# Optimization experiments

Hardware: AMD Instinct MI355X
Metric: run time of the kernel (lower is better)

Reference implementation:

```python
import jax, jax.numpy as jnp
import numpy as np

N_NODES = 100000
N_EDGES = 1600000
D_IN = 128
D_HID = 128
D_PROJ = 128
D_DEC = 512
BN_EPS = 1e-5
ENC_SLOPE = 0.5
DEC_SLOPE = 0.01


def _leaky(x, slope):
    return jnp.where(x >= 0, x, slope * x)


def setup_inputs() -> dict:
    key = jax.random.key(0)
    ks = jax.random.split(key, 12)
    glorot = lambda k, shp: jax.random.normal(k, shp, jnp.float32) * (1.0 / np.sqrt(shp[-1]))
    return {
        "x": jax.random.normal(ks[0], (N_NODES, D_IN), jnp.float32),
        "edge_index": jax.random.randint(ks[1], (2, N_EDGES), 0, N_NODES, jnp.int64),
        # SAGEConv: lin_l (neighbor aggr, with bias), lin_r (root, no bias)
        "Wl": glorot(ks[2], (D_HID, D_IN)),
        "bl": jnp.zeros((D_HID,), jnp.float32),
        "Wr": glorot(ks[3], (D_HID, D_IN)),
        # projection head: Linear + PReLU
        "Wp": glorot(ks[4], (D_PROJ, D_HID)),
        "bp": jnp.zeros((D_PROJ,), jnp.float32),
        "a_prelu": jnp.asarray(0.25, jnp.float32),
        # decoder: Linear -> BN -> LeakyReLU -> Linear
        "Wd1": glorot(ks[5], (D_DEC, D_HID)),
        "bd1": jnp.zeros((D_DEC,), jnp.float32),
        "gamma": jnp.ones((D_DEC,), jnp.float32),
        "beta": jnp.zeros((D_DEC,), jnp.float32),
        "Wd2": glorot(ks[6], (D_IN, D_DEC)),
        "bd2": jnp.zeros((D_IN,), jnp.float32),
    }


def reference(x, edge_index, Wl, bl, Wr, Wp, bp, a_prelu, Wd1, bd1, gamma, beta, Wd2, bd2):
    n = x.shape[0]
    src, dst = edge_index[0], edge_index[1]
    # SAGEConv mean aggregation: gather source features, segment-mean at dst
    msg_sum = jax.ops.segment_sum(x[src], dst, num_segments=n)   # [N, D_IN]
    cnt = jax.ops.segment_sum(jnp.ones((src.shape[0],), x.dtype), dst, num_segments=n)
    aggr = msg_sum / jnp.maximum(cnt, 1.0)[:, None]              # isolated nodes -> 0
    h = aggr @ Wl.T + bl + x @ Wr.T                              # lin_l(aggr) + lin_r(x)
    h = _leaky(h, ENC_SLOPE)                                     # encoder LeakyReLU(0.5)
    # projection head: Linear + PReLU
    zp = h @ Wp.T + bp
    z = jnp.where(zp >= 0, zp, a_prelu * zp)
    # decoder: Linear -> BatchNorm1d (training batch stats, biased var) -> LeakyReLU -> Linear
    d = h @ Wd1.T + bd1
    mu = jnp.mean(d, axis=0)
    var = jnp.mean(jnp.square(d - mu), axis=0)
    d = (d - mu) * jax.lax.rsqrt(var + BN_EPS) * gamma + beta
    d = _leaky(d, DEC_SLOPE)
    rec = d @ Wd2.T + bd2
    target = x
    return (h, z, rec, target)
```

## Files before the change

### kernel.cpp

```cpp
#include <hip/hip_runtime.h>
#include <cstdint>
#include <cstddef>

#define D 128
#define DDEC 512

typedef __attribute__((ext_vector_type(8))) short short8;
typedef __attribute__((ext_vector_type(4))) float f32x4;

__device__ __forceinline__ ushort f2bf(float f) {
  uint32_t u = __float_as_uint(f);
  u = u + 0x7FFF + ((u >> 16) & 1);
  return (ushort)(u >> 16);
}
__device__ __forceinline__ float bf2f(ushort u) {
  return __uint_as_float(((uint32_t)u) << 16);
}

__global__ void detect_i64(const int* __restrict__ ei, int* __restrict__ flag) {
  if (threadIdx.x == 0 && blockIdx.x == 0) {
    int allz = 1;
    for (int k = 0; k < 64; ++k)
      if (ei[2 * k + 1] != 0) { allz = 0; break; }
    *flag = allz ? 2 : 1;
  }
}

__global__ __launch_bounds__(256) void prep_count_kernel(
    const float* __restrict__ x, const float* __restrict__ Wl,
    const float* __restrict__ Wr, const float* __restrict__ Wp,
    const float* __restrict__ Wd1, const float* __restrict__ Wd2,
    const int* __restrict__ ei,
    ushort* __restrict__ xb, ushort* __restrict__ wb,
    float* __restrict__ tgt,
    int* __restrict__ deg, const int* __restrict__ flag,
    int n8, int xblocks, int E)
{
  int b = blockIdx.x;
  if (b < xblocks) {
    int i = b * 256 + threadIdx.x;
    if (i >= n8) return;
    const float* s = x + (size_t)i * 8;
    float4 f0 = *(const float4*)s;
    float4 f1 = *(const float4*)(s + 4);
    short8 v;
    v[0] = (short)f2bf(f0.x); v[1] = (short)f2bf(f0.y);
    v[2] = (short)f2bf(f0.z); v[3] = (short)f2bf(f0.w);
    v[4] = (short)f2bf(f1.x); v[5] = (short)f2bf(f1.y);
    v[6] = (short)f2bf(f1.z); v[7] = (short)f2bf(f1.w);
    *(short8*)&xb[(size_t)i * 8] = v;
    if (tgt) {
      *(float4*)&tgt[(size_t)i * 8] = f0;
      *(float4*)&tgt[(size_t)i * 8 + 4] = f1;
    }
  } else if (b < xblocks + 704) {
    int i = (b - xblocks) * 256 + threadIdx.x;
    if (i >= 180224) return;
    float v;
    if (i < 16384) v = Wl[i];
    else if (i < 32768) v = Wr[i - 16384];
    else if (i < 49152) v = Wp[i - 32768];
    else if (i < 114688) v = Wd1[i - 49152];
    else v = Wd2[i - 114688];
    wb[i] = f2bf(v);
  } else {
    int e = (b - xblocks - 704) * 256 + threadIdx.x;
    if (e >= E) return;
    int s = *flag;
    int dst = ei[((long long)E + e) * s];
    atomicAdd(&deg[dst], 1);
  }
}

__global__ __launch_bounds__(256) void scan_reduce(
    const int* __restrict__ deg, int* __restrict__ bsum, int N)
{
  __shared__ int red[256];
  int base = blockIdx.x * 1024 + threadIdx.x * 4;
  int s = 0;
#pragma unroll
  for (int k = 0; k < 4; ++k) { int i = base + k; if (i < N) s += deg[i]; }
  red[threadIdx.x] = s;
  __syncthreads();
  for (int off = 128; off > 0; off >>= 1) {
    if (threadIdx.x < off) red[threadIdx.x] += red[threadIdx.x + off];
    __syncthreads();
  }
  if (threadIdx.x == 0) bsum[blockIdx.x] = red[0];
}

__global__ void scan_bsum(int* __restrict__ bsum, int* __restrict__ rowptr,
                          int NB, int N, int E)
{
  __shared__ int tmp[256];
  int t = threadIdx.x;
  int v = (t < NB) ? bsum[t] : 0;
  tmp[t] = v;
  __syncthreads();
  for (int off = 1; off < 256; off <<= 1) {
    int add = (t >= off) ? tmp[t - off] : 0;
    __syncthreads();
    tmp[t] += add;
    __syncthreads();
  }
  if (t < NB) bsum[t] = tmp[t] - v;
  if (t == 0) rowptr[N] = E;
}

__global__ __launch_bounds__(256) void scan_final(
    const int* __restrict__ deg, const int* __restrict__ bsum,
    int* __restrict__ rowptr, int N)
{
  __shared__ int tsum[256];
  int base = blockIdx.x * 1024 + threadIdx.x * 4;
  int loc[4]; int s = 0;
#pragma unroll
  for (int k = 0; k < 4; ++k) { int i = base + k; loc[k] = (i < N) ? deg[i] : 0; s += loc[k]; }
  tsum[threadIdx.x] = s;
  __syncthreads();
  for (int off = 1; off < 256; off <<= 1) {
    int add = (threadIdx.x >= off) ? tsum[threadIdx.x - off] : 0;
    __syncthreads();
    tsum[threadIdx.x] += add;
    __syncthreads();
  }
  int excl = tsum[threadIdx.x] - s + bsum[blockIdx.x];
#pragma unroll
  for (int k = 0; k < 4; ++k) {
    int i = base + k;
    if (i < N) { rowptr[i] = excl; excl += loc[k]; }
  }
}

__global__ __launch_bounds__(256) void fill_csr(
    const int* __restrict__ ei, const int* __restrict__ rowptr,
    int* __restrict__ fillc, int* __restrict__ colidx,
    const int* __restrict__ flag, int E)
{
  int e = blockIdx.x * 256 + threadIdx.x;
  if (e >= E) return;
  int s = *flag;
  int src = ei[(long long)e * s];
  int dst = ei[((long long)E + e) * s];
  int pos = rowptr[dst] + atomicAdd(&fillc[dst], 1);
  colidx[pos] = src;
}

__global__ __launch_bounds__(256) void aggregate_kernel(
    const int* __restrict__ rowptr, const int* __restrict__ colidx,
    const ushort* __restrict__ xb, ushort* __restrict__ aggrb, int N)
{
  int wave = (blockIdx.x * 256 + threadIdx.x) >> 6;
  int lane = threadIdx.x & 63;
  if (wave >= N) return;
  int s = rowptr[wave], epos = rowptr[wave + 1];
  float ax = 0.f, ay = 0.f;
  int e = s;
  for (; e + 3 < epos; e += 4) {
    int s0 = colidx[e], s1 = colidx[e + 1], s2 = colidx[e + 2], s3 = colidx[e + 3];
    uint u0 = *(const uint*)&xb[(size_t)s0 * D + lane * 2];
    uint u1 = *(const uint*)&xb[(size_t)s1 * D + lane * 2];
    uint u2 = *(const uint*)&xb[(size_t)s2 * D + lane * 2];
    uint u3 = *(const uint*)&xb[(size_t)s3 * D + lane * 2];
    ax += __uint_as_float(u0 << 16) + __uint_as_float(u1 << 16)
        + __uint_as_float(u2 << 16) + __uint_as_float(u3 << 16);
    ay += __uint_as_float(u0 & 0xFFFF0000u) + __uint_as_float(u1 & 0xFFFF0000u)
        + __uint_as_float(u2 & 0xFFFF0000u) + __uint_as_float(u3 & 0xFFFF0000u);
  }
  for (; e < epos; ++e) {
    uint u0 = *(const uint*)&xb[(size_t)colidx[e] * D + lane * 2];
    ax += __uint_as_float(u0 << 16);
    ay += __uint_as_float(u0 & 0xFFFF0000u);
  }
  int degn = epos - s;
  float inv = 1.0f / (float)(degn > 0 ? degn : 1);
  uint out = ((uint)f2bf(ax * inv)) | (((uint)f2bf(ay * inv)) << 16);
  *(uint*)&aggrb[(size_t)wave * D + lane * 2] = out;
}

__device__ __forceinline__ void mma_tile_g(const ushort* __restrict__ A, size_t ald,
                                           const ushort* __restrict__ B, size_t bld,
                                           f32x4 acc[4][4], int lane)
{
  const int r = lane & 15, g = lane >> 4;
#pragma unroll
  for (int ks = 0; ks < 4; ++ks) {
    short8 a[4], b[4];
#pragma unroll
    for (int m = 0; m < 4; ++m)
      a[m] = *(const short8*)&A[(size_t)(m * 16 + r) * ald + ks * 32 + g * 8];
#pragma unroll
    for (int n = 0; n < 4; ++n)
      b[n] = *(const short8*)&B[(size_t)(n * 16 + r) * bld + ks * 32 + g * 8];
#pragma unroll
    for (int m = 0; m < 4; ++m)
#pragma unroll
      for (int n = 0; n < 4; ++n)
        acc[m][n] = __builtin_amdgcn_mfma_f32_16x16x32_bf16(a[m], b[n], acc[m][n], 0, 0, 0);
  }
}

__device__ __forceinline__ void mma_tile_l(const ushort* aLds,
                                           const ushort* __restrict__ bGlb, size_t bld,
                                           f32x4 acc[4][4], int lane)
{
  const int r = lane & 15, g = lane >> 4;
#pragma unroll
  for (int ks = 0; ks < 4; ++ks) {
    short8 a[4], b[4];
#pragma unroll
    for (int m = 0; m < 4; ++m)
      a[m] = *(const short8*)&aLds[(m * 16 + r) * 136 + ks * 32 + g * 8];
#pragma unroll
    for (int n = 0; n < 4; ++n)
      b[n] = *(const short8*)&bGlb[(size_t)(n * 16 + r) * bld + ks * 32 + g * 8];
#pragma unroll
    for (int m = 0; m < 4; ++m)
#pragma unroll
      for (int n = 0; n < 4; ++n)
        acc[m][n] = __builtin_amdgcn_mfma_f32_16x16x32_bf16(a[m], b[n], acc[m][n], 0, 0, 0);
  }
}

__device__ __forceinline__ void stage128(const float* __restrict__ src, int N,
                                         int row0, ushort* lds, int t)
{
#pragma unroll
  for (int p = 0; p < 8; ++p) {
    int r = (t >> 4) + p * 16;
    int c = (t & 15) * 8;
    short8 v = {};
    int row = row0 + r;
    if (row < N) {
      const float* s = src + (size_t)row * D + c;
      float4 f0 = *(const float4*)s;
      float4 f1 = *(const float4*)(s + 4);
      v[0] = (short)f2bf(f0.x); v[1] = (short)f2bf(f0.y);
      v[2] = (short)f2bf(f0.z); v[3] = (short)f2bf(f0.w);
      v[4] = (short)f2bf(f1.x); v[5] = (short)f2bf(f1.y);
      v[6] = (short)f2bf(f1.z); v[7] = (short)f2bf(f1.w);
    }
    *(short8*)&lds[r * 136 + c] = v;
  }
}

__global__ __launch_bounds__(256, 3) void gemm_h_dstat(
    const ushort* __restrict__ aggrb, const ushort* __restrict__ xb,
    const ushort* __restrict__ Wlb, const ushort* __restrict__ Wrb,
    const ushort* __restrict__ Wd1b, const float* __restrict__ bl,
    float* __restrict__ h, ushort* __restrict__ hb,
    float* __restrict__ sums, float* __restrict__ sumsq, int N)
{
  __shared__ ushort Hs[128 * 136];
  __shared__ float part1[8][132];
  __shared__ float part2[8][132];
  const int t = threadIdx.x;
  const int row0 = blockIdx.x * 128;
  const int lane = t & 63, w = t >> 6;
  const int wm = w >> 1, wn = w & 1;
  const int g = lane >> 4, cr = lane & 15;
  {
    f32x4 acc[4][4] = {};
    mma_tile_g(aggrb + (size_t)(row0 + wm * 64) * D, D, Wlb + (size_t)(wn * 64) * D, D, acc, lane);
    mma_tile_g(xb + (size_t)(row0 + wm * 64) * D, D, Wrb + (size_t)(wn * 64) * D, D, acc, lane);
#pragma unroll
    for (int n = 0; n < 4; ++n) {
      int col = wn * 64 + n * 16 + cr;
      float b = bl[col];
#pragma unroll
      for (int m = 0; m < 4; ++m)
#pragma unroll
        for (int rr = 0; rr < 4; ++rr) {
          int lrow = wm * 64 + m * 16 + g * 4 + rr;
          int row = row0 + lrow;
          float v = acc[m][n][rr] + b;
          v = (v >= 0.f) ? v : 0.5f * v;
          ushort bv = f2bf(v);
          if (row < N) {
            h[(size_t)row * D + col] = v;
            hb[(size_t)row * D + col] = bv;
          }
          Hs[lrow * 136 + col] = bv;
        }
    }
  }
  __syncthreads();
  for (int c0 = 0; c0 < DDEC; c0 += 128) {
    f32x4 dacc[4][4] = {};
    mma_tile_l(Hs + wm * 64 * 136, Wd1b + (size_t)(c0 + wn * 64) * D, D, dacc, lane);
#pragma unroll
    for (int n = 0; n < 4; ++n) {
      float s1 = 0.f, s2 = 0.f;
#pragma unroll
      for (int m = 0; m < 4; ++m)
#pragma unroll
        for (int rr = 0; rr < 4; ++rr) {
          int row = row0 + wm * 64 + m * 16 + g * 4 + rr;
          if (row < N) {
            float v = dacc[m][n][rr];
            s1 += v; s2 += v * v;
          }
        }
      part1[wm * 4 + g][wn * 64 + n * 16 + cr] = s1;
      part2[wm * 4 + g][wn * 64 + n * 16 + cr] = s2;
    }
    __syncthreads();
    if (t < 128) {
      float s = 0;
#pragma unroll
      for (int k = 0; k < 8; ++k) s += part1[k][t];
      atomicAdd(&sums[c0 + t], s);
    } else {
      int c = t - 128;
      float s = 0;
#pragma unroll
      for (int k = 0; k < 8; ++k) s += part2[k][c];
      atomicAdd(&sumsq[c0 + c], s);
    }
    __syncthreads();
  }
}

__global__ void finalize_kernel(
    const float* __restrict__ sums, const float* __restrict__ sumsq,
    const float* __restrict__ gamma, const float* __restrict__ beta,
    float* __restrict__ scale, float* __restrict__ shift, int N)
{
  int c = blockIdx.x * blockDim.x + threadIdx.x;
  if (c < DDEC) {
    float inv_n = 1.0f / (float)N;
    float mu = sums[c] * inv_n;
    float var = sumsq[c] * inv_n - mu * mu;
    float sc = gamma[c] * rsqrtf(var + 1e-5f);
    scale[c] = sc;
    shift[c] = beta[c] - mu * sc;
  }
}

__global__ __launch_bounds__(256, 2) void recz_fused(
    const ushort* __restrict__ hb, const ushort* __restrict__ Wd1b,
    const ushort* __restrict__ Wd2b,
    const float* __restrict__ scale, const float* __restrict__ shift,
    const float* __restrict__ bd2, float* __restrict__ rec,
    const ushort* __restrict__ Wpb, const float* __restrict__ bp,
    const float* __restrict__ ap, float* __restrict__ z, int N, int rb)
{
  __shared__ ushort Hs[128 * 136];
  __shared__ ushort Dn[128 * 136];
  const int t = threadIdx.x;
  const int lane = t & 63, w = t >> 6;
  const int wm = w >> 1, wn = w & 1;
  const int g = lane >> 4, cr = lane & 15;
  if (blockIdx.x < rb) {
    const int row0 = blockIdx.x * 128;
#pragma unroll
    for (int p = 0; p < 8; ++p) {
      int idx = t + p * 256;
      int r = idx >> 4, c = (idx & 15) * 8;
      short8 v = *(const short8*)&hb[(size_t)(row0 + r) * D + c];
      *(short8*)&Hs[r * 136 + c] = v;
    }
    f32x4 acc[4][4] = {};
    __syncthreads();
    for (int c0 = 0; c0 < DDEC; c0 += 128) {
      f32x4 dacc[4][4] = {};
      mma_tile_l(Hs + wm * 64 * 136, Wd1b + (size_t)(c0 + wn * 64) * D, D, dacc, lane);
      __syncthreads();
#pragma unroll
      for (int n = 0; n < 4; ++n) {
        int lc = wn * 64 + n * 16 + cr;
        int c = c0 + lc;
        float sc = scale[c], sh = shift[c];
#pragma unroll
        for (int m = 0; m < 4; ++m)
#pragma unroll
          for (int rr = 0; rr < 4; ++rr) {
            float v = dacc[m][n][rr] * sc + sh;
            v = (v >= 0.f) ? v : 0.01f * v;
            Dn[(wm * 64 + m * 16 + g * 4 + rr) * 136 + lc] = f2bf(v);
          }
      }
      __syncthreads();
      mma_tile_l(Dn + wm * 64 * 136, Wd2b + (size_t)(wn * 64) * DDEC + c0, DDEC, acc, lane);
    }
#pragma unroll
    for (int n = 0; n < 4; ++n) {
      int col = wn * 64 + n * 16 + cr;
      float b = bd2[col];
#pragma unroll
      for (int m = 0; m < 4; ++m)
#pragma unroll
        for (int rr = 0; rr < 4; ++rr) {
          int row = row0 + wm * 64 + m * 16 + g * 4 + rr;
          if (row < N) rec[(size_t)row * D + col] = acc[m][n][rr] + b;
        }
    }
  } else {
    const int row0 = (blockIdx.x - rb) * 128;
    f32x4 acc[4][4] = {};
    mma_tile_g(hb + (size_t)(row0 + wm * 64) * D, D, Wpb + (size_t)(wn * 64) * D, D, acc, lane);
    const float alpha = ap[0];
#pragma unroll
    for (int n = 0; n < 4; ++n) {
      int col = wn * 64 + n * 16 + cr;
      float b = bp[col];
#pragma unroll
      for (int m = 0; m < 4; ++m)
#pragma unroll
        for (int rr = 0; rr < 4; ++rr) {
          int row = row0 + wm * 64 + m * 16 + g * 4 + rr;
          if (row < N) {
            float v = acc[m][n][rr] + b;
            z[(size_t)row * D + col] = (v >= 0.f) ? v : alpha * v;
          }
        }
    }
  }
}

__global__ __launch_bounds__(256, 3) void gemm_h_mfma(
    const ushort* __restrict__ aggrb, const ushort* __restrict__ xb,
    const ushort* __restrict__ Wlb, const ushort* __restrict__ Wrb,
    const float* __restrict__ bl, float* __restrict__ h,
    ushort* __restrict__ hb, int N)
{
  const int t = threadIdx.x;
  const int row0 = blockIdx.x * 128;
  const int lane = t & 63, w = t >> 6;
  const int wm = w >> 1, wn = w & 1;
  f32x4 acc[4][4] = {};
  mma_tile_g(aggrb + (size_t)(row0 + wm * 64) * D, D, Wlb + (size_t)(wn * 64) * D, D, acc, lane);
  mma_tile_g(xb + (size_t)(row0 + wm * 64) * D, D, Wrb + (size_t)(wn * 64) * D, D, acc, lane);
  const int g = lane >> 4, cr = lane & 15;
#pragma unroll
  for (int n = 0; n < 4; ++n) {
    int col = wn * 64 + n * 16 + cr;
    float b = bl[col];
#pragma unroll
    for (int m = 0; m < 4; ++m)
#pragma unroll
      for (int rr = 0; rr < 4; ++rr) {
        int row = row0 + wm * 64 + m * 16 + g * 4 + rr;
        if (row < N) {
          float v = acc[m][n][rr] + b;
          v = (v >= 0.f) ? v : 0.5f * v;
          h[(size_t)row * D + col] = v;
          hb[(size_t)row * D + col] = f2bf(v);
        }
      }
  }
}

__global__ __launch_bounds__(256, 4) void dstat_mfma(
    const ushort* __restrict__ hb, const ushort* __restrict__ Wd1b,
    float* __restrict__ sums, float* __restrict__ sumsq, int N)
{
  __shared__ float part1[8][132];
  __shared__ float part2[8][132];
  const int t = threadIdx.x;
  const int row0 = blockIdx.x * 128;
  const int lane = t & 63, w = t >> 6;
  const int wm = w >> 1, wn = w & 1;
  const int g = lane >> 4, cr = lane & 15;
  for (int c0 = 0; c0 < DDEC; c0 += 128) {
    f32x4 dacc[4][4] = {};
    mma_tile_g(hb + (size_t)(row0 + wm * 64) * D, D,
               Wd1b + (size_t)(c0 + wn * 64) * D, D, dacc, lane);
#pragma unroll
    for (int n = 0; n < 4; ++n) {
      float s1 = 0.f, s2 = 0.f;
#pragma unroll
      for (int m = 0; m < 4; ++m)
#pragma unroll
        for (int rr = 0; rr < 4; ++rr) {
          int row = row0 + wm * 64 + m * 16 + g * 4 + rr;
          if (row < N) {
            float v = dacc[m][n][rr];
            s1 += v; s2 += v * v;
          }
        }
      part1[wm * 4 + g][wn * 64 + n * 16 + cr] = s1;
      part2[wm * 4 + g][wn * 64 + n * 16 + cr] = s2;
    }
    __syncthreads();
    if (t < 128) {
      float s = 0;
#pragma unroll
      for (int k = 0; k < 8; ++k) s += part1[k][t];
      atomicAdd(&sums[c0 + t], s);
    } else {
      int c = t - 128;
      float s = 0;
#pragma unroll
      for (int k = 0; k < 8; ++k) s += part2[k][c];
      atomicAdd(&sumsq[c0 + c], s);
    }
    __syncthreads();
  }
}

__global__ __launch_bounds__(256, 2) void rec_mfma(
    const ushort* __restrict__ hb, const ushort* __restrict__ Wd1b,
    const ushort* __restrict__ Wd2b,
    const float* __restrict__ scale, const float* __restrict__ shift,
    const float* __restrict__ bd2, float* __restrict__ rec, int N)
{
  __shared__ ushort Hs[128 * 136];
  __shared__ ushort Dn[128 * 136];
  const int t = threadIdx.x;
  const int row0 = blockIdx.x * 128;
#pragma unroll
  for (int p = 0; p < 8; ++p) {
    int idx = t + p * 256;
    int r = idx >> 4, c = (idx & 15) * 8;
    short8 v = *(const short8*)&hb[(size_t)(row0 + r) * D + c];
    *(short8*)&Hs[r * 136 + c] = v;
  }
  const int lane = t & 63, w = t >> 6;
  const int wm = w >> 1, wn = w & 1;
  const int g = lane >> 4, cr = lane & 15;
  f32x4 acc[4][4] = {};
  __syncthreads();
  for (int c0 = 0; c0 < DDEC; c0 += 128) {
    f32x4 dacc[4][4] = {};
    mma_tile_l(Hs + wm * 64 * 136, Wd1b + (size_t)(c0 + wn * 64) * D, D, dacc, lane);
    __syncthreads();
#pragma unroll
    for (int n = 0; n < 4; ++n) {
      int lc = wn * 64 + n * 16 + cr;
      int c = c0 + lc;
      float sc = scale[c], sh = shift[c];
#pragma unroll
      for (int m = 0; m < 4; ++m)
#pragma unroll
        for (int rr = 0; rr < 4; ++rr) {
          float v = dacc[m][n][rr] * sc + sh;
          v = (v >= 0.f) ? v : 0.01f * v;
          Dn[(wm * 64 + m * 16 + g * 4 + rr) * 136 + lc] = f2bf(v);
        }
    }
    __syncthreads();
    mma_tile_l(Dn + wm * 64 * 136, Wd2b + (size_t)(wn * 64) * DDEC + c0, DDEC, acc, lane);
  }
#pragma unroll
  for (int n = 0; n < 4; ++n) {
    int col = wn * 64 + n * 16 + cr;
    float b = bd2[col];
#pragma unroll
    for (int m = 0; m < 4; ++m)
#pragma unroll
      for (int rr = 0; rr < 4; ++rr) {
        int row = row0 + wm * 64 + m * 16 + g * 4 + rr;
        if (row < N) rec[(size_t)row * D + col] = acc[m][n][rr] + b;
      }
  }
}

__global__ __launch_bounds__(256, 2) void gemm_z_staged(
    const float* __restrict__ h, const ushort* __restrict__ Wpb,
    const float* __restrict__ bp, const float* __restrict__ ap,
    float* __restrict__ z, int N)
{
  __shared__ ushort As[128 * 136];
  const int t = threadIdx.x;
  const int row0 = blockIdx.x * 128;
  stage128(h, N, row0, As, t);
  __syncthreads();
  const int lane = t & 63, w = t >> 6;
  const int wm = w >> 1, wn = w & 1;
  f32x4 acc[4][4] = {};
  mma_tile_l(As + wm * 64 * 136, Wpb + (size_t)(wn * 64) * D, D, acc, lane);
  const float alpha = ap[0];
  const int g = lane >> 4, cr = lane & 15;
#pragma unroll
  for (int n = 0; n < 4; ++n) {
    int col = wn * 64 + n * 16 + cr;
    float b = bp[col];
#pragma unroll
    for (int m = 0; m < 4; ++m)
#pragma unroll
      for (int rr = 0; rr < 4; ++rr) {
        int row = row0 + wm * 64 + m * 16 + g * 4 + rr;
        if (row < N) {
          float v = acc[m][n][rr] + b;
          z[(size_t)row * D + col] = (v >= 0.f) ? v : alpha * v;
        }
      }
  }
}

extern "C" void kernel_launch(void* const* d_in, const int* in_sizes, int n_in,
                              void* d_out, int out_size, void* d_ws, size_t ws_size,
                              hipStream_t stream)
{
  const float* x   = (const float*)d_in[0];
  const int*   ei  = (const int*)d_in[1];
  const float* Wl  = (const float*)d_in[2];
  const float* bl  = (const float*)d_in[3];
  const float* Wr  = (const float*)d_in[4];
  const float* Wp  = (const float*)d_in[5];
  const float* bp  = (const float*)d_in[6];
  const float* ap  = (const float*)d_in[7];
  const float* Wd1 = (const float*)d_in[8];
  const float* bd1 = (const float*)d_in[9];
  const float* gm  = (const float*)d_in[10];
  const float* bt  = (const float*)d_in[11];
  const float* Wd2 = (const float*)d_in[12];
  const float* bd2 = (const float*)d_in[13];
  (void)bd1;

  const int N = in_sizes[0] / D;
  const int E = in_sizes[1] / 2;

  float* h_out   = (float*)d_out;
  float* z_out   = h_out + (size_t)N * D;
  float* rec_out = z_out + (size_t)N * D;
  float* tgt_out = rec_out + (size_t)N * D;

  const size_t ws_need = ((size_t)3 * N + E + 4096) * 4
                       + (size_t)3 * N * D * 2 + 360448
                       + ((size_t)N + 128) * DDEC * 2 + 2048;
  const bool usews = ws_size >= ws_need;

  int *deg, *fillc, *bsum, *flag, *rowptr, *colidx;
  float *sums, *sumsq, *scale, *shift;
  ushort *xb, *hb, *aggrb, *wb;

  if (usews) {
    deg    = (int*)d_ws;
    fillc  = deg + N;
    sums   = (float*)(fillc + N);
    sumsq  = sums + 512;
    scale  = sumsq + 512;
    shift  = scale + 512;
    bsum   = (int*)(shift + 512);
    flag   = bsum + 256;
    rowptr = flag + 16;
    colidx = rowptr + (N + 16);
    xb     = (ushort*)(((uintptr_t)(colidx + E) + 255) & ~(uintptr_t)255);
    hb     = xb + (size_t)N * D;
    aggrb  = hb + (size_t)N * D;
    wb     = aggrb + (size_t)N * D;
  } else {
    sums   = (float*)d_ws;
    sumsq  = sums + DDEC;
    scale  = sumsq + DDEC;
    shift  = scale + DDEC;
    flag   = (int*)(shift + DDEC);
    bsum   = flag + 1;
    colidx = (int*)tgt_out;
    deg    = colidx + E;
    fillc  = deg + N;
    rowptr = fillc + N;
    xb     = (ushort*)(tgt_out + 2000000);
    wb     = (ushort*)(tgt_out + 8500000);
    aggrb  = (ushort*)z_out;
    hb     = aggrb + (size_t)N * D;
  }
  ushort* Wlb  = wb;
  ushort* Wrb  = wb + 16384;
  ushort* Wpb  = wb + 32768;
  ushort* Wd1b = wb + 49152;
  ushort* Wd2b = wb + 114688;

  if (usews) {
    hipMemsetAsync(deg, 0, (size_t)(2 * N + 1024) * sizeof(int), stream);
  } else {
    hipMemsetAsync(deg, 0, (size_t)2 * N * sizeof(int), stream);
    hipMemsetAsync(sums, 0, (size_t)2 * DDEC * sizeof(float), stream);
  }

  detect_i64<<<1, 64, 0, stream>>>(ei, flag);

  int n8 = N * (D / 8);
  int xblocks = (n8 + 255) / 256;
  int eb = (E + 255) / 256;
  prep_count_kernel<<<xblocks + 704 + eb, 256, 0, stream>>>(
      x, Wl, Wr, Wp, Wd1, Wd2, ei, xb, wb,
      usews ? tgt_out : nullptr, deg, flag, n8, xblocks, E);

  int NB = (N + 1023) / 1024;
  scan_reduce<<<NB, 256, 0, stream>>>(deg, bsum, N);
  scan_bsum<<<1, 256, 0, stream>>>(bsum, rowptr, NB, N, E);
  scan_final<<<NB, 256, 0, stream>>>(deg, bsum, rowptr, N);

  fill_csr<<<eb, 256, 0, stream>>>(ei, rowptr, fillc, colidx, flag, E);

  long long ag_threads = (long long)N * 64;
  aggregate_kernel<<<(int)((ag_threads + 255) / 256), 256, 0, stream>>>(
      rowptr, colidx, xb, aggrb, N);

  int rb = (N + 127) / 128;
  if (usews) {
    gemm_h_dstat<<<rb, 256, 0, stream>>>(aggrb, xb, Wlb, Wrb, Wd1b, bl,
                                         h_out, hb, sums, sumsq, N);
    finalize_kernel<<<2, 256, 0, stream>>>(sums, sumsq, gm, bt, scale, shift, N);
    recz_fused<<<2 * rb, 256, 0, stream>>>(hb, Wd1b, Wd2b, scale, shift, bd2, rec_out,
                                           Wpb, bp, ap, z_out, N, rb);
  } else {
    gemm_h_mfma<<<rb, 256, 0, stream>>>(aggrb, xb, Wlb, Wrb, bl, h_out, hb, N);
    dstat_mfma<<<rb, 256, 0, stream>>>(hb, Wd1b, sums, sumsq, N);
    finalize_kernel<<<2, 256, 0, stream>>>(sums, sumsq, gm, bt, scale, shift, N);
    rec_mfma<<<rb, 256, 0, stream>>>(hb, Wd1b, Wd2b, scale, shift, bd2, rec_out, N);
    gemm_z_staged<<<rb, 256, 0, stream>>>(h_out, Wpb, bp, ap, z_out, N);
    hipMemcpyAsync(tgt_out, x, (size_t)N * D * sizeof(float), hipMemcpyDeviceToDevice, stream);
  }
}
```

Before: 460.4 us.

## Fuse projection head into h/dstat kernel and split-K rec decoder across warps

Computes z from the LDS-resident h tile inside the first GEMM kernel, so the separate projection blocks no longer have to re-read hb. Double-buffers the BN partial-sum scratch so one barrier per chunk can be dropped. Rewrites the rec kernel so each warp owns half of the 512 decoder columns with per-warp LDS staging and no block barriers inside the loop, then reduces the two halves through LDS at the end. The cost is higher register pressure (32 accumulators per lane) and reading Wd1/Wd2 straight from global memory.

After: 722.8 us. 1.57x slower.

```diff
diff --git a/kernel.cpp b/kernel.cpp
--- a/kernel.cpp
+++ b/kernel.cpp
@@ -244,16 +244,18 @@
   }
 }
 
-__global__ __launch_bounds__(256, 3) void gemm_h_dstat(
+__global__ __launch_bounds__(256, 3) void gemm_hz_dstat(
     const ushort* __restrict__ aggrb, const ushort* __restrict__ xb,
     const ushort* __restrict__ Wlb, const ushort* __restrict__ Wrb,
-    const ushort* __restrict__ Wd1b, const float* __restrict__ bl,
-    float* __restrict__ h, ushort* __restrict__ hb,
+    const ushort* __restrict__ Wpb, const ushort* __restrict__ Wd1b,
+    const float* __restrict__ bl, const float* __restrict__ bp,
+    const float* __restrict__ ap,
+    float* __restrict__ h, ushort* __restrict__ hb, float* __restrict__ z,
     float* __restrict__ sums, float* __restrict__ sumsq, int N)
 {
   __shared__ ushort Hs[128 * 136];
-  __shared__ float part1[8][132];
-  __shared__ float part2[8][132];
+  __shared__ float part1[2][8][132];
+  __shared__ float part2[2][8][132];
   const int t = threadIdx.x;
   const int row0 = blockIdx.x * 128;
   const int lane = t & 63, w = t >> 6;
@@ -285,7 +287,29 @@
     }
   }
   __syncthreads();
-  for (int c0 = 0; c0 < DDEC; c0 += 128) {
+  {
+    f32x4 zacc[4][4] = {};
+    mma_tile_l(Hs + wm * 64 * 136, Wpb + (size_t)(wn * 64) * D, D, zacc, lane);
+    const float alpha = ap[0];
+#pragma unroll
+    for (int n = 0; n < 4; ++n) {
+      int col = wn * 64 + n * 16 + cr;
+      float b = bp[col];
+#pragma unroll
+      for (int m = 0; m < 4; ++m)
+#pragma unroll
+        for (int rr = 0; rr < 4; ++rr) {
+          int row = row0 + wm * 64 + m * 16 + g * 4 + rr;
+          if (row < N) {
+            float v = zacc[m][n][rr] + b;
+            z[(size_t)row * D + col] = (v >= 0.f) ? v : alpha * v;
+          }
+        }
+    }
+  }
+  for (int cc = 0; cc < 4; ++cc) {
+    int c0 = cc * 128;
+    int pb = cc & 1;
     f32x4 dacc[4][4] = {};
     mma_tile_l(Hs + wm * 64 * 136, Wd1b + (size_t)(c0 + wn * 64) * D, D, dacc, lane);
 #pragma unroll
@@ -301,23 +325,22 @@
             s1 += v; s2 += v * v;
           }
         }
-      part1[wm * 4 + g][wn * 64 + n * 16 + cr] = s1;
-      part2[wm * 4 + g][wn * 64 + n * 16 + cr] = s2;
+      part1[pb][wm * 4 + g][wn * 64 + n * 16 + cr] = s1;
+      part2[pb][wm * 4 + g][wn * 64 + n * 16 + cr] = s2;
     }
     __syncthreads();
     if (t < 128) {
       float s = 0;
 #pragma unroll
-      for (int k = 0; k < 8; ++k) s += part1[k][t];
+      for (int k = 0; k < 8; ++k) s += part1[pb][k][t];
       atomicAdd(&sums[c0 + t], s);
     } else {
       int c = t - 128;
       float s = 0;
 #pragma unroll
-      for (int k = 0; k < 8; ++k) s += part2[k][c];
+      for (int k = 0; k < 8; ++k) s += part2[pb][k][c];
       atomicAdd(&sumsq[c0 + c], s);
     }
-    __syncthreads();
   }
 }
 
@@ -337,84 +360,105 @@
   }
 }
 
-__global__ __launch_bounds__(256, 2) void recz_fused(
+__global__ __launch_bounds__(256, 2) void rec_v2(
     const ushort* __restrict__ hb, const ushort* __restrict__ Wd1b,
     const ushort* __restrict__ Wd2b,
     const float* __restrict__ scale, const float* __restrict__ shift,
-    const float* __restrict__ bd2, float* __restrict__ rec,
-    const ushort* __restrict__ Wpb, const float* __restrict__ bp,
-    const float* __restrict__ ap, float* __restrict__ z, int N, int rb)
-{
-  __shared__ ushort Hs[128 * 136];
-  __shared__ ushort Dn[128 * 136];
+    const float* __restrict__ bd2, float* __restrict__ rec, int N)
+{
+  __shared__ __align__(16) ushort smem[35840];
+  ushort* Hs = smem;
   const int t = threadIdx.x;
+  const int row0 = blockIdx.x * 128;
+#pragma unroll
+  for (int p = 0; p < 8; ++p) {
+    int idx = t + p * 256;
+    int r = idx >> 4, c = (idx & 15) * 8;
+    short8 v = *(const short8*)&hb[(size_t)(row0 + r) * D + c];
+    *(short8*)&Hs[r * 136 + c] = v;
+  }
+  __syncthreads();
   const int lane = t & 63, w = t >> 6;
-  const int wm = w >> 1, wn = w & 1;
-  const int g = lane >> 4, cr = lane & 15;
-  if (blockIdx.x < rb) {
-    const int row0 = blockIdx.x * 128;
-#pragma unroll
-    for (int p = 0; p < 8; ++p) {
-      int idx = t + p * 256;
-      int r = idx >> 4, c = (idx & 15) * 8;
-      short8 v = *(const short8*)&hb[(size_t)(row0 + r) * D + c];
-      *(short8*)&Hs[r * 136 + c] = v;
-    }
-    f32x4 acc[4][4] = {};
-    __syncthreads();
-    for (int c0 = 0; c0 < DDEC; c0 += 128) {
-      f32x4 dacc[4][4] = {};
-      mma_tile_l(Hs + wm * 64 * 136, Wd1b + (size_t)(c0 + wn * 64) * D, D, dacc, lane);
-      __syncthreads();
-#pragma unroll
-      for (int n = 0; n < 4; ++n) {
-        int lc = wn * 64 + n * 16 + cr;
-        int c = c0 + lc;
-        float sc = scale[c], sh = shift[c];
+  const int wr = (w >> 1) * 64;
+  const int cbase = (w & 1) * 256;
+  ushort* Dn = smem + 17408 + w * 4608;
+  const int r = lane & 15, g = lane >> 4;
+  f32x4 acc[4][8] = {};
+  const ushort* Arow = Hs + wr * 136;
+  for (int cc = 0; cc < 4; ++cc) {
+    const int c0 = cbase + cc * 64;
+    f32x4 dacc[4][4] = {};
+    const ushort* Brow = Wd1b + (size_t)c0 * D;
+#pragma unroll
+    for (int ks = 0; ks < 4; ++ks) {
+      short8 a[4], b[4];
+#pragma unroll
+      for (int m = 0; m < 4; ++m)
+        a[m] = *(const short8*)&Arow[(m * 16 + r) * 136 + ks * 32 + g * 8];
+#pragma unroll
+      for (int n = 0; n < 4; ++n)
+        b[n] = *(const short8*)&Brow[(size_t)(n * 16 + r) * D + ks * 32 + g * 8];
+#pragma unroll
+      for (int m = 0; m < 4; ++m)
+#pragma unroll
+        for (int n = 0; n < 4; ++n)
+          dacc[m][n] = __builtin_amdgcn_mfma_f32_16x16x32_bf16(a[m], b[n], dacc[m][n], 0, 0, 0);
+    }
+#pragma unroll
+    for (int n = 0; n < 4; ++n) {
+      int cg = c0 + n * 16 + r;
+      float sc = scale[cg], sh = shift[cg];
+#pragma unroll
+      for (int m = 0; m < 4; ++m)
+#pragma unroll
+        for (int rr = 0; rr < 4; ++rr) {
+          float v = dacc[m][n][rr] * sc + sh;
+          v = (v >= 0.f) ? v : 0.01f * v;
+          Dn[(m * 16 + g * 4 + rr) * 72 + n * 16 + r] = f2bf(v);
+        }
+    }
+#pragma unroll
+    for (int ks2 = 0; ks2 < 2; ++ks2) {
+      short8 a2[4];
+#pragma unroll
+      for (int m = 0; m < 4; ++m)
+        a2[m] = *(const short8*)&Dn[(m * 16 + r) * 72 + ks2 * 32 + g * 8];
+#pragma unroll
+      for (int n8 = 0; n8 < 8; ++n8) {
+        short8 b2 = *(const short8*)&Wd2b[(size_t)(n8 * 16 + r) * DDEC + c0 + ks2 * 32 + g * 8];
 #pragma unroll
         for (int m = 0; m < 4; ++m)
-#pragma unroll
-          for (int rr = 0; rr < 4; ++rr) {
-            float v = dacc[m][n][rr] * sc + sh;
-            v = (v >= 0.f) ? v : 0.01f * v;
-            Dn[(wm * 64 + m * 16 + g * 4 + rr) * 136 + lc] = f2bf(v);
-          }
+          acc[m][n8] = __builtin_amdgcn_mfma_f32_16x16x32_bf16(a2[m], b2, acc[m][n8], 0, 0, 0);
       }
-      __syncthreads();
-      mma_tile_l(Dn + wm * 64 * 136, Wd2b + (size_t)(wn * 64) * DDEC + c0, DDEC, acc, lane);
-    }
-#pragma unroll
-    for (int n = 0; n < 4; ++n) {
-      int col = wn * 64 + n * 16 + cr;
-      float b = bd2[col];
-#pragma unroll
-      for (int m = 0; m < 4; ++m)
-#pragma unroll
-        for (int rr = 0; rr < 4; ++rr) {
-          int row = row0 + wm * 64 + m * 16 + g * 4 + rr;
-          if (row < N) rec[(size_t)row * D + col] = acc[m][n][rr] + b;
-        }
-    }
-  } else {
-    const int row0 = (blockIdx.x - rb) * 128;
-    f32x4 acc[4][4] = {};
-    mma_tile_g(hb + (size_t)(row0 + wm * 64) * D, D, Wpb + (size_t)(wn * 64) * D, D, acc, lane);
-    const float alpha = ap[0];
-#pragma unroll
-    for (int n = 0; n < 4; ++n) {
-      int col = wn * 64 + n * 16 + cr;
-      float b = bp[col];
-#pragma unroll
-      for (int m = 0; m < 4; ++m)
-#pragma unroll
-        for (int rr = 0; rr < 4; ++rr) {
-          int row = row0 + wm * 64 + m * 16 + g * 4 + rr;
-          if (row < N) {
-            float v = acc[m][n][rr] + b;
-            z[(size_t)row * D + col] = (v >= 0.f) ? v : alpha * v;
-          }
-        }
-    }
+    }
+  }
+  __syncthreads();
+  float* dump = (float*)smem + (size_t)w * 4096;
+  const int ndump0 = (w & 1) ? 0 : 4;
+#pragma unroll
+  for (int nn = 0; nn < 4; ++nn)
+#pragma unroll
+    for (int m = 0; m < 4; ++m)
+#pragma unroll
+      for (int rr = 0; rr < 4; ++rr)
+        dump[((nn * 4 + m) * 4 + rr) * 64 + lane] = acc[m][ndump0 + nn][rr];
+  __syncthreads();
+  const float* pdump = (const float*)smem + (size_t)(w ^ 1) * 4096;
+  const int nstore0 = (w & 1) ? 4 : 0;
+#pragma unroll
+  for (int nn = 0; nn < 4; ++nn) {
+    int n = nstore0 + nn;
+    int col = n * 16 + r;
+    float b = bd2[col];
+#pragma unroll
+    for (int m = 0; m < 4; ++m)
+#pragma unroll
+      for (int rr = 0; rr < 4; ++rr) {
+        int row = row0 + wr + m * 16 + g * 4 + rr;
+        if (row < N)
+          rec[(size_t)row * D + col] =
+              acc[m][n][rr] + pdump[((nn * 4 + m) * 4 + rr) * 64 + lane] + b;
+      }
   }
 }
 
@@ -692,11 +736,11 @@
 
   int rb = (N + 127) / 128;
   if (usews) {
-    gemm_h_dstat<<<rb, 256, 0, stream>>>(aggrb, xb, Wlb, Wrb, Wd1b, bl,
-                                         h_out, hb, sums, sumsq, N);
+    gemm_hz_dstat<<<rb, 256, 0, stream>>>(aggrb, xb, Wlb, Wrb, Wpb, Wd1b,
+                                          bl, bp, ap, h_out, hb, z_out,
+                                          sums, sumsq, N);
     finalize_kernel<<<2, 256, 0, stream>>>(sums, sumsq, gm, bt, scale, shift, N);
-    recz_fused<<<2 * rb, 256, 0, stream>>>(hb, Wd1b, Wd2b, scale, shift, bd2, rec_out,
-                                           Wpb, bp, ap, z_out, N, rb);
+    rec_v2<<<rb, 256, 0, stream>>>(hb, Wd1b, Wd2b, scale, shift, bd2, rec_out, N);
   } else {
     gemm_h_mfma<<<rb, 256, 0, stream>>>(aggrb, xb, Wlb, Wrb, bl, h_out, hb, N);
     dstat_mfma<<<rb, 256, 0, stream>>>(hb, Wd1b, sums, sumsq, N);
```
